# Kernel tuning notes

Hardware: AMD Instinct MI355X
Metric: run time of the kernel (lower is better)

The kernel has to match this reference:

```python
import jax, jax.numpy as jnp
import numpy as np

ENC_DIM, DEC_DIM, ATT_DIM = 2048, 512, 512

def setup_inputs() -> dict:
    key = jax.random.key(0)
    ks = jax.random.split(key, 8)
    s_enc = 1.0 / np.sqrt(ENC_DIM)
    s_dec = 1.0 / np.sqrt(DEC_DIM)
    s_att = 1.0 / np.sqrt(ATT_DIM)
    return {
        "encoder_out": jax.random.normal(ks[0], (256, 196, ENC_DIM), jnp.float32),
        "decoder_hidden": jax.random.normal(ks[1], (256, DEC_DIM), jnp.float32),
        "W_enc": jax.random.uniform(ks[2], (ENC_DIM, ATT_DIM), jnp.float32, -s_enc, s_enc),
        "b_enc": jax.random.uniform(ks[3], (ATT_DIM,), jnp.float32, -s_enc, s_enc),
        "W_dec": jax.random.uniform(ks[4], (DEC_DIM, ATT_DIM), jnp.float32, -s_dec, s_dec),
        "b_dec": jax.random.uniform(ks[5], (ATT_DIM,), jnp.float32, -s_dec, s_dec),
        "W_att": jax.random.uniform(ks[6], (ATT_DIM, 1), jnp.float32, -s_att, s_att),
        "b_att": jax.random.uniform(ks[7], (1,), jnp.float32, -s_att, s_att),
    }

def reference(encoder_out, decoder_hidden, W_enc, b_enc, W_dec, b_dec, W_att, b_att):
    # att1: (B, P, A); att2: (B, 1, A)
    att1 = jnp.einsum('bpe,ea->bpa', encoder_out, W_enc) + b_enc
    att2 = (decoder_hidden @ W_dec + b_dec)[:, None, :]
    # scalar score per pixel: (B, P)
    e = (jax.nn.relu(att1 + att2) @ W_att)[..., 0] + b_att[0]
    alpha = jax.nn.softmax(e, axis=-1)  # softmax over pixels
    z = jnp.einsum('bpe,bp->be', encoder_out, alpha)
    return (z, alpha)
```

## Files before the change

### kernel.cpp

```cpp
#include <hip/hip_runtime.h>
#include <hip/hip_bf16.h>

#define ENC_DIM 2048
#define DEC_DIM 512
#define ATT_DIM 512
#define NB 256
#define NP 196
#define M_TOT (NB * NP)
#define BM 64
#define BK 64
#define NSTEP (ENC_DIM / BK)

typedef __attribute__((ext_vector_type(8))) short short8;
typedef __attribute__((ext_vector_type(4))) float f32x4;

__global__ __launch_bounds__(256) void prep_btt(const float* __restrict__ W,
                                                __hip_bfloat16* __restrict__ Btt) {
    const int gid = blockIdx.x * 256 + threadIdx.x;
    const int kg = gid & 3;
    const int n  = (gid >> 2) & 511;
    const int J  = gid >> 11;
    const int k  = J * 32 + kg * 8;
    union { short8 v; __hip_bfloat16 h[8]; } u;
    #pragma unroll
    for (int i = 0; i < 8; ++i)
        u.h[i] = __float2bfloat16(W[(size_t)(k + i) * ATT_DIM + n]);
    *(short8*)((short*)Btt + (size_t)gid * 8) = u.v;
}

__global__ __launch_bounds__(256) void att2_kernel(const float* __restrict__ dec,
                                                   const float* __restrict__ W_dec,
                                                   const float* __restrict__ b_dec,
                                                   const float* __restrict__ b_enc,
                                                   float* __restrict__ att2f) {
    __shared__ float ds[DEC_DIM];
    const int b = blockIdx.x;
    const int t = threadIdx.x;
    ds[t]       = dec[(size_t)b * DEC_DIM + t];
    ds[t + 256] = dec[(size_t)b * DEC_DIM + t + 256];
    __syncthreads();
    #pragma unroll
    for (int j = 0; j < 2; ++j) {
        const int n = t + j * 256;
        float s = 0.f;
        #pragma unroll 8
        for (int k = 0; k < DEC_DIM; ++k)
            s += ds[k] * W_dec[(size_t)k * ATT_DIM + n];
        att2f[(size_t)b * ATT_DIM + n] = s + b_dec[n] + b_enc[n];
    }
}

__device__ __forceinline__ short8 cvt8v(f32x4 x, f32x4 y) {
    union { short8 v; __hip_bfloat16 h[8]; } u;
    u.h[0] = __float2bfloat16(x[0]);
    u.h[1] = __float2bfloat16(x[1]);
    u.h[2] = __float2bfloat16(x[2]);
    u.h[3] = __float2bfloat16(x[3]);
    u.h[4] = __float2bfloat16(y[0]);
    u.h[5] = __float2bfloat16(y[1]);
    u.h[6] = __float2bfloat16(y[2]);
    u.h[7] = __float2bfloat16(y[3]);
    return u.v;
}

__global__ __launch_bounds__(512, 4) void e_kernel(const float* __restrict__ enc,
                                                   const short* __restrict__ Btt,
                                                   const float* __restrict__ att2f,
                                                   const float* __restrict__ W_att,
                                                   float* __restrict__ e_out) {
    const int tid  = threadIdx.x;
    const int lane = tid & 63;
    const int wv   = tid >> 6;
    const int l15  = lane & 15;
    const int kg   = lane >> 4;
    const int M0   = blockIdx.x * BM;

    __shared__ __attribute__((aligned(16))) short Asm[2][8][64][8];
    __shared__ float ebuf[8][64];

    const int m_s = tid >> 3;
    const int c_s = tid & 7;
    const float* pa = enc + (size_t)(M0 + m_s) * ENC_DIM + c_s * 8;

    const short* pb = Btt + (wv * 64 + l15) * 32 + kg * 8;

    f32x4 acc[4][4];
    #pragma unroll
    for (int i = 0; i < 4; ++i)
        #pragma unroll
        for (int j = 0; j < 4; ++j)
            acc[i][j] = (f32x4){0.f, 0.f, 0.f, 0.f};

    {
        f32x4 g0 = *(const f32x4*)pa;
        f32x4 g1 = *(const f32x4*)(pa + 4);
        *(short8*)&Asm[0][c_s][m_s ^ c_s][0] = cvt8v(g0, g1);
    }

    for (int step = 0; step < NSTEP; ++step) {
        const int cur = step & 1;
        f32x4 g0, g1;
        if (step + 1 < NSTEP) {
            g0 = *(const f32x4*)(pa + (step + 1) * BK);
            g1 = *(const f32x4*)(pa + (step + 1) * BK + 4);
        }
        __syncthreads();
        const short* pbs = pb + (size_t)step * 32768;
        #pragma unroll
        for (int j = 0; j < 2; ++j) {
            const short8 b0 = *(const short8*)(pbs + j * 16384 + 0 * 512);
            const short8 b1 = *(const short8*)(pbs + j * 16384 + 1 * 512);
            const short8 b2 = *(const short8*)(pbs + j * 16384 + 2 * 512);
            const short8 b3 = *(const short8*)(pbs + j * 16384 + 3 * 512);
            const int kb = j * 4 + kg;
            const short8 a0 = *(const short8*)&Asm[cur][kb][(0 * 16 + l15) ^ kb][0];
            const short8 a1 = *(const short8*)&Asm[cur][kb][(1 * 16 + l15) ^ kb][0];
            const short8 a2 = *(const short8*)&Asm[cur][kb][(2 * 16 + l15) ^ kb][0];
            const short8 a3 = *(const short8*)&Asm[cur][kb][(3 * 16 + l15) ^ kb][0];
            acc[0][0] = __builtin_amdgcn_mfma_f32_16x16x32_bf16(a0, b0, acc[0][0], 0, 0, 0);
            acc[0][1] = __builtin_amdgcn_mfma_f32_16x16x32_bf16(a0, b1, acc[0][1], 0, 0, 0);
            acc[0][2] = __builtin_amdgcn_mfma_f32_16x16x32_bf16(a0, b2, acc[0][2], 0, 0, 0);
            acc[0][3] = __builtin_amdgcn_mfma_f32_16x16x32_bf16(a0, b3, acc[0][3], 0, 0, 0);
            acc[1][0] = __builtin_amdgcn_mfma_f32_16x16x32_bf16(a1, b0, acc[1][0], 0, 0, 0);
            acc[1][1] = __builtin_amdgcn_mfma_f32_16x16x32_bf16(a1, b1, acc[1][1], 0, 0, 0);
            acc[1][2] = __builtin_amdgcn_mfma_f32_16x16x32_bf16(a1, b2, acc[1][2], 0, 0, 0);
            acc[1][3] = __builtin_amdgcn_mfma_f32_16x16x32_bf16(a1, b3, acc[1][3], 0, 0, 0);
            acc[2][0] = __builtin_amdgcn_mfma_f32_16x16x32_bf16(a2, b0, acc[2][0], 0, 0, 0);
            acc[2][1] = __builtin_amdgcn_mfma_f32_16x16x32_bf16(a2, b1, acc[2][1], 0, 0, 0);
            acc[2][2] = __builtin_amdgcn_mfma_f32_16x16x32_bf16(a2, b2, acc[2][2], 0, 0, 0);
            acc[2][3] = __builtin_amdgcn_mfma_f32_16x16x32_bf16(a2, b3, acc[2][3], 0, 0, 0);
            acc[3][0] = __builtin_amdgcn_mfma_f32_16x16x32_bf16(a3, b0, acc[3][0], 0, 0, 0);
            acc[3][1] = __builtin_amdgcn_mfma_f32_16x16x32_bf16(a3, b1, acc[3][1], 0, 0, 0);
            acc[3][2] = __builtin_amdgcn_mfma_f32_16x16x32_bf16(a3, b2, acc[3][2], 0, 0, 0);
            acc[3][3] = __builtin_amdgcn_mfma_f32_16x16x32_bf16(a3, b3, acc[3][3], 0, 0, 0);
        }
        if (step + 1 < NSTEP) {
            *(short8*)&Asm[cur ^ 1][c_s][m_s ^ c_s][0] = cvt8v(g0, g1);
        }
    }

    float wat[4];
    #pragma unroll
    for (int nf = 0; nf < 4; ++nf) wat[nf] = W_att[wv * 64 + nf * 16 + l15];

    #pragma unroll
    for (int mf = 0; mf < 4; ++mf) {
        #pragma unroll
        for (int r = 0; r < 4; ++r) {
            const int ml = mf * 16 + kg * 4 + r;
            const int bb = (M0 + ml) / NP;
            const float* arow = att2f + (size_t)bb * ATT_DIM + wv * 64 + l15;
            float s = 0.f;
            #pragma unroll
            for (int nf = 0; nf < 4; ++nf) {
                float v = acc[mf][nf][r] + arow[nf * 16];
                s += fmaxf(v, 0.f) * wat[nf];
            }
            s += __shfl_xor(s, 1);
            s += __shfl_xor(s, 2);
            s += __shfl_xor(s, 4);
            s += __shfl_xor(s, 8);
            if (l15 == 0) ebuf[wv][ml] = s;
        }
    }
    __syncthreads();
    if (tid < 64) {
        float s = 0.f;
        #pragma unroll
        for (int w = 0; w < 8; ++w) s += ebuf[w][tid];
        e_out[M0 + tid] = s;
    }
}

__global__ __launch_bounds__(256) void z_kernel(const float* __restrict__ enc,
                                                const float* __restrict__ e,
                                                float* __restrict__ z,
                                                float* __restrict__ alpha) {
    const int b  = blockIdx.x;
    const int cb = blockIdx.y;
    const int t  = threadIdx.x;
    __shared__ float al[NP];
    __shared__ float red[4];

    float ev = (t < NP) ? e[(size_t)b * NP + t] : -1e30f;
    float m = ev;
    #pragma unroll
    for (int o = 32; o > 0; o >>= 1) m = fmaxf(m, __shfl_xor(m, o));
    if ((t & 63) == 0) red[t >> 6] = m;
    __syncthreads();
    m = fmaxf(fmaxf(red[0], red[1]), fmaxf(red[2], red[3]));
    __syncthreads();
    float ex = (t < NP) ? __expf(ev - m) : 0.f;
    float s = ex;
    #pragma unroll
    for (int o = 32; o > 0; o >>= 1) s += __shfl_xor(s, o);
    if ((t & 63) == 0) red[t >> 6] = s;
    __syncthreads();
    s = red[0] + red[1] + red[2] + red[3];
    const float a = ex * (1.0f / s);
    if (t < NP) {
        al[t] = a;
        if (cb == 0) alpha[(size_t)b * NP + t] = a;
    }
    __syncthreads();

    const int c0 = cb * 1024 + t * 4;
    const float4* ep = (const float4*)(enc + (size_t)b * NP * ENC_DIM + c0);
    float4 zv = make_float4(0.f, 0.f, 0.f, 0.f);
    #pragma unroll 4
    for (int p = 0; p < NP; ++p) {
        const float ap = al[p];
        const float4 v = ep[(size_t)p * (ENC_DIM / 4)];
        zv.x += ap * v.x;
        zv.y += ap * v.y;
        zv.z += ap * v.z;
        zv.w += ap * v.w;
    }
    *(float4*)(z + (size_t)b * ENC_DIM + c0) = zv;
}

extern "C" void kernel_launch(void* const* d_in, const int* in_sizes, int n_in,
                              void* d_out, int out_size, void* d_ws, size_t ws_size,
                              hipStream_t stream) {
    const float* enc   = (const float*)d_in[0];
    const float* dec   = (const float*)d_in[1];
    const float* W_enc = (const float*)d_in[2];
    const float* b_enc = (const float*)d_in[3];
    const float* W_dec = (const float*)d_in[4];
    const float* b_dec = (const float*)d_in[5];
    const float* W_att = (const float*)d_in[6];

    float* z     = (float*)d_out;
    float* alpha = z + (size_t)NB * ENC_DIM;

    char* ws = (char*)d_ws;
    __hip_bfloat16* Btt = (__hip_bfloat16*)ws;
    float* att2f        = (float*)(ws + 2 * 1024 * 1024);
    float* e            = (float*)(ws + 2 * 1024 * 1024 + 512 * 1024);

    prep_btt<<<512, 256, 0, stream>>>(W_enc, Btt);
    att2_kernel<<<NB, 256, 0, stream>>>(dec, W_dec, b_dec, b_enc, att2f);
    e_kernel<<<M_TOT / BM, 512, 0, stream>>>(enc, (const short*)Btt, att2f, W_att, e);
    z_kernel<<<dim3(NB, 2), 256, 0, stream>>>(enc, e, z, alpha);
}
```

Baseline: 309.8 us.

## Stage fp32 encoder tiles via direct global-to-LDS loads and retile MFMA warps

The GEMM kernel now loads fp32 encoder tiles straight into LDS with global_load_lds and an XOR swizzle, converting to bf16 when reading fragments, instead of converting in registers before the LDS store. Warps are retiled 2x4 so each holds 2x8 accumulators, and occupancy is lowered to 2 blocks per CU. The two prep kernels are merged into one launch, and the z reduction uses two accumulators. The intent is to cut register staging and B-fragment reloads in exchange for twice the LDS footprint and more conversion work per fragment read.

```diff
diff --git a/kernel.cpp b/kernel.cpp
--- a/kernel.cpp
+++ b/kernel.cpp
@@ -14,39 +14,46 @@
 typedef __attribute__((ext_vector_type(8))) short short8;
 typedef __attribute__((ext_vector_type(4))) float f32x4;
 
-__global__ __launch_bounds__(256) void prep_btt(const float* __restrict__ W,
-                                                __hip_bfloat16* __restrict__ Btt) {
-    const int gid = blockIdx.x * 256 + threadIdx.x;
-    const int kg = gid & 3;
-    const int n  = (gid >> 2) & 511;
-    const int J  = gid >> 11;
-    const int k  = J * 32 + kg * 8;
-    union { short8 v; __hip_bfloat16 h[8]; } u;
-    #pragma unroll
-    for (int i = 0; i < 8; ++i)
-        u.h[i] = __float2bfloat16(W[(size_t)(k + i) * ATT_DIM + n]);
-    *(short8*)((short*)Btt + (size_t)gid * 8) = u.v;
-}
-
-__global__ __launch_bounds__(256) void att2_kernel(const float* __restrict__ dec,
+__device__ __forceinline__ void gll16(const float* g, float* l) {
+    __builtin_amdgcn_global_load_lds((const __attribute__((address_space(1))) void*)g,
+                                     (__attribute__((address_space(3))) void*)l,
+                                     16, 0, 0);
+}
+
+__global__ __launch_bounds__(256) void prep_kernel(const float* __restrict__ W,
+                                                   __hip_bfloat16* __restrict__ Btt,
+                                                   const float* __restrict__ dec,
                                                    const float* __restrict__ W_dec,
                                                    const float* __restrict__ b_dec,
                                                    const float* __restrict__ b_enc,
                                                    float* __restrict__ att2f) {
     __shared__ float ds[DEC_DIM];
-    const int b = blockIdx.x;
-    const int t = threadIdx.x;
-    ds[t]       = dec[(size_t)b * DEC_DIM + t];
-    ds[t + 256] = dec[(size_t)b * DEC_DIM + t + 256];
-    __syncthreads();
-    #pragma unroll
-    for (int j = 0; j < 2; ++j) {
-        const int n = t + j * 256;
-        float s = 0.f;
-        #pragma unroll 8
-        for (int k = 0; k < DEC_DIM; ++k)
-            s += ds[k] * W_dec[(size_t)k * ATT_DIM + n];
-        att2f[(size_t)b * ATT_DIM + n] = s + b_dec[n] + b_enc[n];
+    if (blockIdx.x < 512) {
+        const int gid = blockIdx.x * 256 + threadIdx.x;
+        const int kg = gid & 3;
+        const int n  = (gid >> 2) & 511;
+        const int J  = gid >> 11;
+        const int k  = J * 32 + kg * 8;
+        union { short8 v; __hip_bfloat16 h[8]; } u;
+        #pragma unroll
+        for (int i = 0; i < 8; ++i)
+            u.h[i] = __float2bfloat16(W[(size_t)(k + i) * ATT_DIM + n]);
+        *(short8*)((short*)Btt + (size_t)gid * 8) = u.v;
+    } else {
+        const int b = blockIdx.x - 512;
+        const int t = threadIdx.x;
+        ds[t]       = dec[(size_t)b * DEC_DIM + t];
+        ds[t + 256] = dec[(size_t)b * DEC_DIM + t + 256];
+        __syncthreads();
+        #pragma unroll
+        for (int j = 0; j < 2; ++j) {
+            const int n = t + j * 256;
+            float s = 0.f;
+            #pragma unroll 8
+            for (int k = 0; k < DEC_DIM; ++k)
+                s += ds[k] * W_dec[(size_t)k * ATT_DIM + n];
+            att2f[(size_t)b * ATT_DIM + n] = s + b_dec[n] + b_enc[n];
+        }
     }
 }
 
@@ -63,7 +70,7 @@
     return u.v;
 }
 
-__global__ __launch_bounds__(512, 4) void e_kernel(const float* __restrict__ enc,
+__global__ __launch_bounds__(512, 2) void e_kernel(const float* __restrict__ enc,
                                                    const short* __restrict__ Btt,
                                                    const float* __restrict__ att2f,
                                                    const float* __restrict__ W_att,
@@ -71,105 +78,99 @@
     const int tid  = threadIdx.x;
     const int lane = tid & 63;
     const int wv   = tid >> 6;
+    const int wm   = wv >> 2;
+    const int wn   = wv & 3;
     const int l15  = lane & 15;
     const int kg   = lane >> 4;
     const int M0   = blockIdx.x * BM;
 
-    __shared__ __attribute__((aligned(16))) short Asm[2][8][64][8];
-    __shared__ float ebuf[8][64];
-
-    const int m_s = tid >> 3;
-    const int c_s = tid & 7;
-    const float* pa = enc + (size_t)(M0 + m_s) * ENC_DIM + c_s * 8;
-
-    const short* pb = Btt + (wv * 64 + l15) * 32 + kg * 8;
-
-    f32x4 acc[4][4];
-    #pragma unroll
-    for (int i = 0; i < 4; ++i)
-        #pragma unroll
-        for (int j = 0; j < 4; ++j)
+    __shared__ __attribute__((aligned(16))) float Asm[2][64 * 64];
+    __shared__ float ebuf[4][64];
+
+    const int r0 = wv * 4 + (lane >> 4);
+    const int c16s = lane & 15;
+    const float* src0 = enc + (size_t)(M0 + r0) * ENC_DIM + ((c16s ^ ((r0 & 3) << 1)) << 2);
+    const int r1 = r0 + 32;
+    const float* src1 = enc + (size_t)(M0 + r1) * ENC_DIM + ((c16s ^ ((r1 & 3) << 1)) << 2);
+    float* dst0 = &Asm[0][0] + (size_t)(wv * 64 + lane) * 4;
+    float* dst1 = dst0 + 512 * 4;
+
+    const short* pb = Btt + (wn * 128 + l15) * 32 + kg * 8;
+
+    f32x4 acc[2][8];
+    #pragma unroll
+    for (int i = 0; i < 2; ++i)
+        #pragma unroll
+        for (int j = 0; j < 8; ++j)
             acc[i][j] = (f32x4){0.f, 0.f, 0.f, 0.f};
 
-    {
-        f32x4 g0 = *(const f32x4*)pa;
-        f32x4 g1 = *(const f32x4*)(pa + 4);
-        *(short8*)&Asm[0][c_s][m_s ^ c_s][0] = cvt8v(g0, g1);
-    }
-
+    gll16(src0, dst0);
+    gll16(src1, dst1);
+    __syncthreads();
+
+    int cur = 0;
     for (int step = 0; step < NSTEP; ++step) {
-        const int cur = step & 1;
-        f32x4 g0, g1;
         if (step + 1 < NSTEP) {
-            g0 = *(const f32x4*)(pa + (step + 1) * BK);
-            g1 = *(const f32x4*)(pa + (step + 1) * BK + 4);
+            const int koff = (step + 1) * BK;
+            float* d0 = &Asm[cur ^ 1][0] + (size_t)(wv * 64 + lane) * 4;
+            gll16(src0 + koff, d0);
+            gll16(src1 + koff, d0 + 512 * 4);
+        }
+        const short* pbs = pb + (size_t)step * 32768;
+        const float* As = &Asm[cur][0];
+        #pragma unroll
+        for (int kh = 0; kh < 2; ++kh) {
+            short8 bf[8];
+            #pragma unroll
+            for (int nf = 0; nf < 8; ++nf)
+                bf[nf] = *(const short8*)(pbs + kh * 16384 + nf * 512);
+            short8 af[2];
+            #pragma unroll
+            for (int mf = 0; mf < 2; ++mf) {
+                const int r = wm * 32 + mf * 16 + l15;
+                const int u0 = (kh * 8 + kg * 2) ^ ((r & 3) << 1);
+                const float* lp = As + r * 64 + u0 * 4;
+                f32x4 x = *(const f32x4*)lp;
+                f32x4 y = *(const f32x4*)(lp + 4);
+                af[mf] = cvt8v(x, y);
+            }
+            #pragma unroll
+            for (int mf = 0; mf < 2; ++mf)
+                #pragma unroll
+                for (int nf = 0; nf < 8; ++nf)
+                    acc[mf][nf] = __builtin_amdgcn_mfma_f32_16x16x32_bf16(af[mf], bf[nf], acc[mf][nf], 0, 0, 0);
         }
         __syncthreads();
-        const short* pbs = pb + (size_t)step * 32768;
-        #pragma unroll
-        for (int j = 0; j < 2; ++j) {
-            const short8 b0 = *(const short8*)(pbs + j * 16384 + 0 * 512);
-            const short8 b1 = *(const short8*)(pbs + j * 16384 + 1 * 512);
-            const short8 b2 = *(const short8*)(pbs + j * 16384 + 2 * 512);
-            const short8 b3 = *(const short8*)(pbs + j * 16384 + 3 * 512);
-            const int kb = j * 4 + kg;
-            const short8 a0 = *(const short8*)&Asm[cur][kb][(0 * 16 + l15) ^ kb][0];
-            const short8 a1 = *(const short8*)&Asm[cur][kb][(1 * 16 + l15) ^ kb][0];
-            const short8 a2 = *(const short8*)&Asm[cur][kb][(2 * 16 + l15) ^ kb][0];
-            const short8 a3 = *(const short8*)&Asm[cur][kb][(3 * 16 + l15) ^ kb][0];
-            acc[0][0] = __builtin_amdgcn_mfma_f32_16x16x32_bf16(a0, b0, acc[0][0], 0, 0, 0);
-            acc[0][1] = __builtin_amdgcn_mfma_f32_16x16x32_bf16(a0, b1, acc[0][1], 0, 0, 0);
-            acc[0][2] = __builtin_amdgcn_mfma_f32_16x16x32_bf16(a0, b2, acc[0][2], 0, 0, 0);
-            acc[0][3] = __builtin_amdgcn_mfma_f32_16x16x32_bf16(a0, b3, acc[0][3], 0, 0, 0);
-            acc[1][0] = __builtin_amdgcn_mfma_f32_16x16x32_bf16(a1, b0, acc[1][0], 0, 0, 0);
-            acc[1][1] = __builtin_amdgcn_mfma_f32_16x16x32_bf16(a1, b1, acc[1][1], 0, 0, 0);
-            acc[1][2] = __builtin_amdgcn_mfma_f32_16x16x32_bf16(a1, b2, acc[1][2], 0, 0, 0);
-            acc[1][3] = __builtin_amdgcn_mfma_f32_16x16x32_bf16(a1, b3, acc[1][3], 0, 0, 0);
-            acc[2][0] = __builtin_amdgcn_mfma_f32_16x16x32_bf16(a2, b0, acc[2][0], 0, 0, 0);
-            acc[2][1] = __builtin_amdgcn_mfma_f32_16x16x32_bf16(a2, b1, acc[2][1], 0, 0, 0);
-            acc[2][2] = __builtin_amdgcn_mfma_f32_16x16x32_bf16(a2, b2, acc[2][2], 0, 0, 0);
-            acc[2][3] = __builtin_amdgcn_mfma_f32_16x16x32_bf16(a2, b3, acc[2][3], 0, 0, 0);
-            acc[3][0] = __builtin_amdgcn_mfma_f32_16x16x32_bf16(a3, b0, acc[3][0], 0, 0, 0);
-            acc[3][1] = __builtin_amdgcn_mfma_f32_16x16x32_bf16(a3, b1, acc[3][1], 0, 0, 0);
-            acc[3][2] = __builtin_amdgcn_mfma_f32_16x16x32_bf16(a3, b2, acc[3][2], 0, 0, 0);
-            acc[3][3] = __builtin_amdgcn_mfma_f32_16x16x32_bf16(a3, b3, acc[3][3], 0, 0, 0);
-        }
-        if (step + 1 < NSTEP) {
-            *(short8*)&Asm[cur ^ 1][c_s][m_s ^ c_s][0] = cvt8v(g0, g1);
-        }
-    }
-
-    float wat[4];
-    #pragma unroll
-    for (int nf = 0; nf < 4; ++nf) wat[nf] = W_att[wv * 64 + nf * 16 + l15];
-
-    #pragma unroll
-    for (int mf = 0; mf < 4; ++mf) {
-        #pragma unroll
-        for (int r = 0; r < 4; ++r) {
-            const int ml = mf * 16 + kg * 4 + r;
+        cur ^= 1;
+    }
+
+    float wat[8];
+    #pragma unroll
+    for (int nf = 0; nf < 8; ++nf) wat[nf] = W_att[wn * 128 + nf * 16 + l15];
+
+    #pragma unroll
+    for (int mf = 0; mf < 2; ++mf) {
+        #pragma unroll
+        for (int rr = 0; rr < 4; ++rr) {
+            const int ml = wm * 32 + mf * 16 + kg * 4 + rr;
             const int bb = (M0 + ml) / NP;
-            const float* arow = att2f + (size_t)bb * ATT_DIM + wv * 64 + l15;
+            const float* arow = att2f + (size_t)bb * ATT_DIM + wn * 128 + l15;
             float s = 0.f;
             #pragma unroll
-            for (int nf = 0; nf < 4; ++nf) {
-                float v = acc[mf][nf][r] + arow[nf * 16];
+            for (int nf = 0; nf < 8; ++nf) {
+                float v = acc[mf][nf][rr] + arow[nf * 16];
                 s += fmaxf(v, 0.f) * wat[nf];
             }
             s += __shfl_xor(s, 1);
             s += __shfl_xor(s, 2);
             s += __shfl_xor(s, 4);
             s += __shfl_xor(s, 8);
-            if (l15 == 0) ebuf[wv][ml] = s;
-        }
-    }
-    __syncthreads();
-    if (tid < 64) {
-        float s = 0.f;
-        #pragma unroll
-        for (int w = 0; w < 8; ++w) s += ebuf[w][tid];
-        e_out[M0 + tid] = s;
-    }
+            if (l15 == 0) ebuf[wn][ml] = s;
+        }
+    }
+    __syncthreads();
+    if (tid < 64)
+        e_out[M0 + tid] = ebuf[0][tid] + ebuf[1][tid] + ebuf[2][tid] + ebuf[3][tid];
 }
 
 __global__ __launch_bounds__(256) void z_kernel(const float* __restrict__ enc,
@@ -206,17 +207,19 @@
 
     const int c0 = cb * 1024 + t * 4;
     const float4* ep = (const float4*)(enc + (size_t)b * NP * ENC_DIM + c0);
-    float4 zv = make_float4(0.f, 0.f, 0.f, 0.f);
+    float4 z0 = make_float4(0.f, 0.f, 0.f, 0.f);
+    float4 z1 = make_float4(0.f, 0.f, 0.f, 0.f);
     #pragma unroll 4
-    for (int p = 0; p < NP; ++p) {
-        const float ap = al[p];
-        const float4 v = ep[(size_t)p * (ENC_DIM / 4)];
-        zv.x += ap * v.x;
-        zv.y += ap * v.y;
-        zv.z += ap * v.z;
-        zv.w += ap * v.w;
-    }
-    *(float4*)(z + (size_t)b * ENC_DIM + c0) = zv;
+    for (int p = 0; p < NP; p += 2) {
+        const float a0 = al[p];
+        const float a1 = al[p + 1];
+        const float4 v0 = ep[(size_t)p * (ENC_DIM / 4)];
+        const float4 v1 = ep[(size_t)(p + 1) * (ENC_DIM / 4)];
+        z0.x += a0 * v0.x; z0.y += a0 * v0.y; z0.z += a0 * v0.z; z0.w += a0 * v0.w;
+        z1.x += a1 * v1.x; z1.y += a1 * v1.y; z1.z += a1 * v1.z; z1.w += a1 * v1.w;
+    }
+    z0.x += z1.x; z0.y += z1.y; z0.z += z1.z; z0.w += z1.w;
+    *(float4*)(z + (size_t)b * ENC_DIM + c0) = z0;
 }
 
 extern "C" void kernel_launch(void* const* d_in, const int* in_sizes, int n_in,
@@ -238,8 +241,7 @@
     float* att2f        = (float*)(ws + 2 * 1024 * 1024);
     float* e            = (float*)(ws + 2 * 1024 * 1024 + 512 * 1024);
 
-    prep_btt<<<512, 256, 0, stream>>>(W_enc, Btt);
-    att2_kernel<<<NB, 256, 0, stream>>>(dec, W_dec, b_dec, b_enc, att2f);
+    prep_kernel<<<768, 256, 0, stream>>>(W_enc, Btt, dec, W_dec, b_dec, b_enc, att2f);
     e_kernel<<<M_TOT / BM, 512, 0, stream>>>(enc, (const short*)Btt, att2f, W_att, e);
     z_kernel<<<dim3(NB, 2), 256, 0, stream>>>(enc, e, z, alpha);
 }
```

New measurement: 455.8 us. 1.47x slower.
